# Kernel tuning notes

Hardware: AMD Instinct MI355X
Metric: run time of the kernel (lower is better)

Reference implementation:

```python
import jax, jax.numpy as jnp
import numpy as np

D = 512
K = 32
B = 2
L = 2048


def setup_inputs() -> dict:
    key = jax.random.key(0)
    ks = jax.random.split(key, 12)
    s = 1.0 / np.sqrt(D)
    return {
        "x": jax.random.normal(ks[0], (B, L, D), dtype=jnp.float32),
        "W1": jax.random.normal(ks[1], (D, D), dtype=jnp.float32) * s,
        "b1": jnp.zeros((D,), jnp.float32),
        "W2": jax.random.normal(ks[2], (D, K), dtype=jnp.float32) * s,
        "b2": jnp.zeros((K,), jnp.float32),
        "pos_scale": jnp.array([0.5], jnp.float32),
        "content_scale": jnp.array([0.5], jnp.float32),
        "Wv": jax.random.normal(ks[3], (D, D), dtype=jnp.float32) * s,
        "bv": jnp.zeros((D,), jnp.float32),
        "ln_g": jnp.ones((D,), jnp.float32),
        "ln_b": jnp.zeros((D,), jnp.float32),
        "Wo": jax.random.normal(ks[4], (D, D), dtype=jnp.float32) * s,
        "bo": jnp.zeros((D,), jnp.float32),
    }


def reference(x, W1, b1, W2, b2, pos_scale, content_scale, Wv, bv, ln_g, ln_b, Wo, bo):
    Bb, Ll, Dd = x.shape
    Kk = W2.shape[1]
    # fixed positional phases: outer(positions, 1/10000^(k/K))
    freqs = 1.0 / (10000.0 ** (jnp.arange(Kk, dtype=jnp.float32) / Kk))
    pos_phase = jnp.arange(Ll, dtype=jnp.float32)[:, None] * freqs[None, :]  # [L,K]
    # content phase: Linear -> Tanh -> Linear, then tanh * pi
    h = jnp.tanh(x @ W1 + b1)
    content_phase = jnp.tanh(h @ W2 + b2) * jnp.pi  # [B,L,K]
    total_phase = pos_scale * pos_phase[None] + content_scale * content_phase  # [B,L,K]
    value = x @ Wv + bv  # [B,L,D]
    c = jnp.cos(total_phase)
    s = jnp.sin(total_phase)
    # phasor outer-product bind: [B,L,K,D]
    bound_real = c[..., None] * value[:, :, None, :]
    bound_imag = s[..., None] * value[:, :, None, :]
    mem_real = jnp.cumsum(bound_real, axis=1)
    mem_imag = jnp.cumsum(bound_imag, axis=1)
    retrieved = (mem_real * c[..., None] + mem_imag * s[..., None]).sum(axis=2)  # [B,L,D]
    norm = jnp.sqrt(jnp.arange(1, Ll + 1, dtype=jnp.float32) * Kk)[None, :, None]
    retrieved = retrieved / norm
    # to_out: LayerNorm then Linear
    mu = retrieved.mean(axis=-1, keepdims=True)
    var = retrieved.var(axis=-1, keepdims=True)
    ln = (retrieved - mu) / jnp.sqrt(var + 1e-5) * ln_g + ln_b
    return x + ln @ Wo + bo
```

## Files before the change

### kernel.cpp

```cpp
#include <hip/hip_runtime.h>
#include <hip/hip_bf16.h>
#include <math.h>

#define BB   2
#define LL   2048
#define DD   512
#define KK   32
#define BL   (BB*LL)
#define NCH  64

typedef unsigned short ushort_t;
typedef __bf16 bf16x8 __attribute__((ext_vector_type(8)));
typedef float  f32x4  __attribute__((ext_vector_type(4)));
typedef unsigned short ushort8 __attribute__((ext_vector_type(8)));

__device__ __forceinline__ void gl_lds16(const void* g, void* l) {
    __builtin_amdgcn_global_load_lds(
        (const __attribute__((address_space(1))) void*)g,
        (__attribute__((address_space(3))) void*)l, 16, 0, 0);
}
__device__ __forceinline__ ushort_t f2b(float f) {
    __bf16 b = (__bf16)f; return *(ushort_t*)&b;
}
__device__ __forceinline__ float b2f(ushort_t u) {
    unsigned int x = ((unsigned int)u) << 16; return *(float*)&x;
}

__global__ __launch_bounds__(256) void prep(const float* __restrict__ W1,
                                            const float* __restrict__ Wv,
                                            const float* __restrict__ Wo,
                                            const float* __restrict__ W2,
                                            const float* __restrict__ x,
                                            const float* __restrict__ lng,
                                            const float* __restrict__ lnb,
                                            const float* __restrict__ bo,
                                            __hip_bfloat16* __restrict__ Wct,
                                            __hip_bfloat16* __restrict__ Wot,
                                            __hip_bfloat16* __restrict__ W2T,
                                            __hip_bfloat16* __restrict__ xb,
                                            float* __restrict__ Upart,
                                            float* __restrict__ Vpart)
{
    __shared__ float tile[32][33];
    const int bz = blockIdx.z;
    const int tx = threadIdx.x, ty = threadIdx.y;
    const int t = ty * 32 + tx;

    if (bz == 3) {
        const int bid = blockIdx.y * 16 + blockIdx.x;
        const float4* src = (const float4*)x + (size_t)bid * 2048 + t;
        ushort4* dst = (ushort4*)xb + (size_t)bid * 2048 + t;
        #pragma unroll
        for (int i = 0; i < 8; ++i) {
            float4 v = src[i * 256];
            ushort4 o = {f2b(v.x), f2b(v.y), f2b(v.z), f2b(v.w)};
            dst[i * 256] = o;
        }
        return;
    }
    if (bz == 4) {
        if (blockIdx.x != 0) return;
        const int kg = blockIdx.y;
        const int k0 = kg * 32;
        float u0 = 0.f, u1 = 0.f, v0 = 0.f, v1 = 0.f;
        #pragma unroll 4
        for (int k = 0; k < 32; ++k) {
            const float g1 = lng[k0 + k], b1v = lnb[k0 + k];
            const float w0 = Wo[(size_t)(k0 + k) * 512 + t];
            const float w1 = Wo[(size_t)(k0 + k) * 512 + t + 256];
            u0 = fmaf(g1, w0, u0);  u1 = fmaf(g1, w1, u1);
            v0 = fmaf(b1v, w0, v0); v1 = fmaf(b1v, w1, v1);
        }
        if (kg == 0) { v0 += bo[t]; v1 += bo[t + 256]; }
        Upart[kg * 512 + t] = u0;       Upart[kg * 512 + t + 256] = u1;
        Vpart[kg * 512 + t] = v0;       Vpart[kg * 512 + t + 256] = v1;
        return;
    }
    if (bz == 5) {
        if (blockIdx.x != 0) return;
        const int r0 = blockIdx.y * 32;
        #pragma unroll
        for (int i = 0; i < 4; ++i)
            tile[ty + 8 * i][tx] = W2[(size_t)(r0 + ty + 8 * i) * 32 + tx];
        __syncthreads();
        #pragma unroll
        for (int i = 0; i < 4; ++i)
            W2T[(size_t)(ty + 8 * i) * 512 + r0 + tx] =
                __float2bfloat16(tile[tx][ty + 8 * i]);
        return;
    }
    const float* src = bz == 0 ? W1 : (bz == 1 ? Wv : Wo);
    __hip_bfloat16* dst = bz == 0 ? Wct
                        : (bz == 1 ? Wct + 512 * 512 : Wot);
    const int r0 = blockIdx.y * 32, c0 = blockIdx.x * 32;
    #pragma unroll
    for (int i = 0; i < 4; ++i)
        tile[ty + 8 * i][tx] = src[(size_t)(r0 + ty + 8 * i) * 512 + c0 + tx];
    __syncthreads();
    const float sc = (bz == 2) ? lng[r0 + tx] : 1.f;
    #pragma unroll
    for (int i = 0; i < 4; ++i)
        dst[(size_t)(c0 + ty + 8 * i) * 512 + r0 + tx] =
            __float2bfloat16(tile[tx][ty + 8 * i] * sc);
}

template<int BM, int MODE>
__global__ __launch_bounds__(256) void gemm_mfma(
    const ushort_t* __restrict__ A, const ushort_t* __restrict__ Bt,
    const float* __restrict__ bias0, const float* __restrict__ bias1,
    const float* __restrict__ resid,
    __hip_bfloat16* __restrict__ outH, __hip_bfloat16* __restrict__ outV,
    float* __restrict__ outF, const float* __restrict__ stats)
{
    constexpr int WROWS = BM / 2;
    constexpr int MF    = WROWS / 16;
    constexpr int ACH   = BM / 32;
    __shared__ __align__(16) ushort_t As[BM * 64];
    __shared__ __align__(16) ushort_t Bs[128 * 64];
    __shared__ float muL[BM], rsL[BM], uL[128], vbL[128];

    const int t  = threadIdx.x;
    const int m0 = blockIdx.y * BM, n0 = blockIdx.x * 128;
    const int l  = t & 63, w = t >> 6;
    const int wr = w >> 1, wc = w & 1;
    const int l15 = l & 15, hi = l >> 4;

    if (MODE == 1) {
        if (t < BM) {
            float4 st = *(const float4*)(stats + (size_t)(m0 + t) * 4);
            float s = st.x + st.z, s2 = st.y + st.w;
            float mu = s * (1.f / 512), var = s2 * (1.f / 512) - mu * mu;
            muL[t] = mu;
            rsL[t] = rsqrtf(var + 1e-5f);
        }
        if (t < 128) {
            float u = 0.f, v = 0.f;
            #pragma unroll
            for (int kg = 0; kg < 16; ++kg) {
                u += bias0[kg * 512 + n0 + t];
                v += bias1[kg * 512 + n0 + t];
            }
            uL[t] = u; vbL[t] = v;
        }
    }

    const ushort_t* agp[ACH];
    const ushort_t* bgp[4];
    #pragma unroll
    for (int i = 0; i < ACH; ++i) {
        int row = (t >> 3) + 32 * i, slot = (t & 7) ^ (row & 7);
        agp[i] = A + (size_t)(m0 + row) * 512 + slot * 8;
    }
    #pragma unroll
    for (int i = 0; i < 4; ++i) {
        int row = (t >> 3) + 32 * i, slot = (t & 7) ^ (row & 7);
        bgp[i] = Bt + (size_t)(n0 + row) * 512 + slot * 8;
    }

    int aoff[MF][2], boff[4][2];
    #pragma unroll
    for (int mi = 0; mi < MF; ++mi)
        #pragma unroll
        for (int kh = 0; kh < 2; ++kh) {
            int row = wr * WROWS + mi * 16 + l15;
            aoff[mi][kh] = row * 128 + (((kh * 4 + hi) ^ (row & 7)) * 16);
        }
    #pragma unroll
    for (int nj = 0; nj < 4; ++nj)
        #pragma unroll
        for (int kh = 0; kh < 2; ++kh) {
            int row = wc * 64 + nj * 16 + l15;
            boff[nj][kh] = row * 128 + (((kh * 4 + hi) ^ (row & 7)) * 16);
        }

    f32x4 acc[MF][4];
    #pragma unroll
    for (int mi = 0; mi < MF; ++mi)
        #pragma unroll
        for (int nj = 0; nj < 4; ++nj)
            acc[mi][nj] = f32x4{0.f, 0.f, 0.f, 0.f};

    for (int k0 = 0; k0 < 512; k0 += 64) {
        __syncthreads();
        #pragma unroll
        for (int i = 0; i < ACH; ++i)
            gl_lds16(agp[i] + k0, (char*)As + (size_t)(i * 256 + t) * 16);
        #pragma unroll
        for (int i = 0; i < 4; ++i)
            gl_lds16(bgp[i] + k0, (char*)Bs + (size_t)(i * 256 + t) * 16);
        __syncthreads();
        #pragma unroll
        for (int kh = 0; kh < 2; ++kh) {
            bf16x8 af[MF], bfr[4];
            #pragma unroll
            for (int mi = 0; mi < MF; ++mi)
                af[mi] = *(const bf16x8*)((const char*)As + aoff[mi][kh]);
            #pragma unroll
            for (int nj = 0; nj < 4; ++nj)
                bfr[nj] = *(const bf16x8*)((const char*)Bs + boff[nj][kh]);
            #pragma unroll
            for (int mi = 0; mi < MF; ++mi)
                #pragma unroll
                for (int nj = 0; nj < 4; ++nj)
                    acc[mi][nj] = __builtin_amdgcn_mfma_f32_16x16x32_bf16(
                        af[mi], bfr[nj], acc[mi][nj], 0, 0, 0);
        }
    }

    #pragma unroll
    for (int nj = 0; nj < 4; ++nj) {
        const int gcol = n0 + wc * 64 + nj * 16 + l15;
        if (MODE == 0) {
            const float bsv = (gcol < 512) ? bias0[gcol] : bias1[gcol - 512];
            #pragma unroll
            for (int mi = 0; mi < MF; ++mi)
                #pragma unroll
                for (int r = 0; r < 4; ++r) {
                    const int grow = m0 + wr * WROWS + mi * 16 + hi * 4 + r;
                    float v = acc[mi][nj][r] + bsv;
                    if (gcol < 512)
                        outH[(size_t)grow * 512 + gcol] = __float2bfloat16(tanhf(v));
                    else
                        outV[(size_t)grow * 512 + (gcol - 512)] = __float2bfloat16(v);
                }
        } else {
            const int lc = wc * 64 + nj * 16 + l15;
            const float uN = uL[lc], vbN = vbL[lc];
            #pragma unroll
            for (int mi = 0; mi < MF; ++mi)
                #pragma unroll
                for (int r = 0; r < 4; ++r) {
                    const int rl = wr * WROWS + mi * 16 + hi * 4 + r;
                    const int grow = m0 + rl;
                    const float rs = rsL[rl], mu = muL[rl];
                    outF[(size_t)grow * 512 + gcol] =
                        resid[(size_t)grow * 512 + gcol]
                        + rs * acc[mi][nj][r] - rs * mu * uN + vbN;
                }
        }
    }
}

__global__ __launch_bounds__(256) void scanA(const __hip_bfloat16* __restrict__ Vb,
                                             const __hip_bfloat16* __restrict__ Hb,
                                             const __hip_bfloat16* __restrict__ W2T,
                                             const float* __restrict__ b2,
                                             const float* __restrict__ ps_p,
                                             const float* __restrict__ cs_p,
                                             ushort_t* __restrict__ CSg,
                                             ushort_t* __restrict__ PPg)
{
    __shared__ __align__(16) ushort_t regA[32 * 520];
    __shared__ __align__(16) ushort_t regB[32 * 520];
    ushort_t* Hs  = regA;
    ushort_t* VT  = regA;
    ushort_t* CT  = regA + 256 * 40;
    ushort_t* ST  = regA + 256 * 40 + 32 * 40;
    ushort_t* CSs = regA + 256 * 40 + 2 * 32 * 40;
    ushort_t* W2L = regB;
    ushort_t* PPs = regB;

    const int t = threadIdx.x;
    const int bch = blockIdx.x, dh = blockIdx.y;
    const int b = bch >> 6, ch = bch & 63;
    const size_t vbase = ((size_t)b * LL + ch * 32) * DD + dh * 256;
    const int w = t >> 6, l = t & 63, l15 = l & 15, hi = l >> 4;

    {
        const ushort8* hsrc = (const ushort8*)((const ushort_t*)Hb
                               + ((size_t)b * LL + ch * 32) * DD);
        const ushort8* wsrc = (const ushort8*)((const ushort_t*)W2T);
        #pragma unroll
        for (int i = 0; i < 8; ++i) {
            const int id = i * 256 + t;
            const int row = id >> 6, c8 = id & 63;
            ushort8 hv = hsrc[id];
            ushort8 wv = wsrc[id];
            *(ushort8*)&Hs[row * 520 + c8 * 8] = hv;
            *(ushort8*)&W2L[row * 520 + c8 * 8] = wv;
        }
    }
    __syncthreads();

    f32x4 pacc[2][2];
    #pragma unroll
    for (int mt = 0; mt < 2; ++mt)
        #pragma unroll
        for (int nt = 0; nt < 2; ++nt)
            pacc[mt][nt] = f32x4{0.f,0.f,0.f,0.f};
    for (int ks = 0; ks < 16; ++ks) {
        bf16x8 af[2], bfr[2];
        #pragma unroll
        for (int mt = 0; mt < 2; ++mt)
            af[mt] = *(const bf16x8*)&Hs[(16 * mt + l15) * 520 + ks * 32 + hi * 8];
        #pragma unroll
        for (int nt = 0; nt < 2; ++nt)
            bfr[nt] = *(const bf16x8*)&W2L[(16 * nt + l15) * 520 + ks * 32 + hi * 8];
        #pragma unroll
        for (int mt = 0; mt < 2; ++mt)
            #pragma unroll
            for (int nt = 0; nt < 2; ++nt)
                pacc[mt][nt] = __builtin_amdgcn_mfma_f32_16x16x32_bf16(
                    af[mt], bfr[nt], pacc[mt][nt], 0, 0, 0);
    }
    __syncthreads();

    {
        const float psv = ps_p[0], csv = cs_p[0];
        #pragma unroll
        for (int nt = 0; nt < 2; ++nt) {
            const int kk = l15 + 16 * nt;
            const float freq = exp2f(-(float)kk * (13.287712379549449f / (float)KK));
            const float b2k = b2[kk];
            #pragma unroll
            for (int mt = 0; mt < 2; ++mt) {
                ushort_t cw[4], sw[4];
                #pragma unroll
                for (int r = 0; r < 4; ++r) {
                    const int lloc = 16 * mt + hi * 4 + r;
                    const int lpos = ch * 32 + lloc;
                    const float content = tanhf(pacc[mt][nt][r] + b2k)
                                          * 3.14159265358979323846f * csv;
                    const float total = psv * ((float)lpos * freq) + content;
                    float sv, cv;
                    sincosf(total, &sv, &cv);
                    cw[r] = f2b(cv); sw[r] = f2b(sv);
                    if (dh == 0) {
                        CSs[lloc * 64 + (((kk >> 3) ^ (lloc & 7)) << 3) + (kk & 7)] = cw[r];
                        CSs[lloc * 64 + ((((kk >> 3) + 4) ^ (lloc & 7)) << 3) + (kk & 7)] = sw[r];
                    }
                }
                *(ushort4*)&CT[kk * 40 + 16 * mt + hi * 4] = *(ushort4*)cw;
                *(ushort4*)&ST[kk * 40 + 16 * mt + hi * 4] = *(ushort4*)sw;
            }
        }
    }
    {
        const int lg = t >> 5, dg = t & 31;
        ushort8 r[4];
        #pragma unroll
        for (int i = 0; i < 4; ++i)
            r[i] = *(const ushort8*)((const ushort_t*)Vb + vbase
                                     + (size_t)(lg * 4 + i) * DD + dg * 8);
        #pragma unroll
        for (int jd = 0; jd < 8; ++jd) {
            ushort4 w4 = {r[0][jd], r[1][jd], r[2][jd], r[3][jd]};
            *(ushort4*)&VT[(dg * 8 + jd) * 40 + lg * 4] = w4;
        }
    }
    __syncthreads();

    if (dh == 0) {
        ushort_t* cso = CSg + ((size_t)b * NCH + ch) * 2048;
        *(ushort8*)(cso + t * 8) = *(const ushort8*)&CSs[t * 8];
    }

    bf16x8 afc[2], afs[2];
    #pragma unroll
    for (int mt = 0; mt < 2; ++mt) {
        afc[mt] = *(const bf16x8*)&CT[(l15 + 16 * mt) * 40 + hi * 8];
        afs[mt] = *(const bf16x8*)&ST[(l15 + 16 * mt) * 40 + hi * 8];
    }
    f32x4 aPR[2][4], aPI[2][4];
    #pragma unroll
    for (int mt = 0; mt < 2; ++mt)
        #pragma unroll
        for (int nt = 0; nt < 4; ++nt) {
            aPR[mt][nt] = f32x4{0.f,0.f,0.f,0.f};
            aPI[mt][nt] = f32x4{0.f,0.f,0.f,0.f};
        }
    #pragma unroll
    for (int nt = 0; nt < 4; ++nt) {
        bf16x8 bv = *(const bf16x8*)&VT[(w * 64 + nt * 16 + l15) * 40 + hi * 8];
        #pragma unroll
        for (int mt = 0; mt < 2; ++mt) {
            aPR[mt][nt] = __builtin_amdgcn_mfma_f32_16x16x32_bf16(afc[mt], bv, aPR[mt][nt], 0,0,0);
            aPI[mt][nt] = __builtin_amdgcn_mfma_f32_16x16x32_bf16(afs[mt], bv, aPI[mt][nt], 0,0,0);
        }
    }
    #pragma unroll
    for (int mt = 0; mt < 2; ++mt)
        #pragma unroll
        for (int nt = 0; nt < 4; ++nt) {
            const int dloc = w * 64 + nt * 16 + l15;
            const int kq = 16 * mt + hi * 4;
            const int oR = kq >> 3, oI = 4 + (kq >> 3);
            const int sub = (hi & 1) * 4;
            ushort4 pr4 = {f2b(aPR[mt][nt][0]), f2b(aPR[mt][nt][1]),
                           f2b(aPR[mt][nt][2]), f2b(aPR[mt][nt][3])};
            ushort4 pi4 = {f2b(aPI[mt][nt][0]), f2b(aPI[mt][nt][1]),
                           f2b(aPI[mt][nt][2]), f2b(aPI[mt][nt][3])};
            *(ushort4*)&PPs[dloc * 64 + ((oR ^ (dloc & 7)) * 8) + sub] = pr4;
            *(ushort4*)&PPs[dloc * 64 + ((oI ^ (dloc & 7)) * 8) + sub] = pi4;
        }
    __syncthreads();
    ushort_t* gout = PPg + ((size_t)bch * 512 + dh * 256) * 64;
    #pragma unroll
    for (int i = 0; i < 8; ++i)
        *(ushort8*)(gout + (size_t)(i * 256 + t) * 8) =
            *(const ushort8*)&PPs[(i * 256 + t) * 8];
}

__global__ __launch_bounds__(256) void scan_prefix(ushort_t* __restrict__ PPg)
{
    const int g = blockIdx.x * 256 + threadIdx.x;
    const int b = g >> 15, p = g & 32767;
    float run = 0.f;
    for (int gg = 0; gg < 4; ++gg) {
        ushort_t v[16];
        #pragma unroll
        for (int i = 0; i < 16; ++i)
            v[i] = PPg[(size_t)(b * 64 + gg * 16 + i) * 32768 + p];
        #pragma unroll
        for (int i = 0; i < 16; ++i) {
            ushort_t o = f2b(run);
            run += b2f(v[i]);
            PPg[(size_t)(b * 64 + gg * 16 + i) * 32768 + p] = o;
        }
    }
}

__global__ __launch_bounds__(256) void scanC(__hip_bfloat16* Vb,
                                             const ushort_t* __restrict__ CSg,
                                             const ushort_t* __restrict__ PPg,
                                             float* __restrict__ StatsG)
{
    __shared__ __align__(16) ushort_t VT[256 * 40];
    __shared__ __align__(16) ushort_t PPT[256 * 64];
    __shared__ __align__(16) ushort_t CS[32 * 64];
    __shared__ __align__(16) ushort_t G[32 * 40];
    __shared__ __align__(16) ushort_t RT[4][32 * 64];
    __shared__ float2 statsL[4][32];

    const int t = threadIdx.x;
    const int bch = blockIdx.x, dh = blockIdx.y;
    const int b = bch >> 6, ch = bch & 63;
    const size_t vbase = ((size_t)b * LL + ch * 32) * DD + dh * 256;

    {
        const ushort_t* ppg = PPg + ((size_t)bch * 512 + dh * 256) * 64;
        #pragma unroll
        for (int i = 0; i < 8; ++i)
            gl_lds16(ppg + (size_t)(i * 256 + t) * 8,
                     (char*)PPT + (size_t)(i * 256 + t) * 16);
        const ushort_t* csg = CSg + ((size_t)b * NCH + ch) * 2048;
        gl_lds16(csg + (size_t)t * 8, (char*)CS + (size_t)t * 16);
    }
    {
        const int lg = t >> 5, dg = t & 31;
        ushort8 r[4];
        #pragma unroll
        for (int i = 0; i < 4; ++i)
            r[i] = *(const ushort8*)((const ushort_t*)Vb + vbase
                                     + (size_t)(lg * 4 + i) * DD + dg * 8);
        #pragma unroll
        for (int jd = 0; jd < 8; ++jd) {
            ushort4 w4 = {r[0][jd], r[1][jd], r[2][jd], r[3][jd]};
            *(ushort4*)&VT[(dg * 8 + jd) * 40 + lg * 4] = w4;
        }
    }
    __syncthreads();

    const int w = t >> 6, l = t & 63, l15 = l & 15, hi = l >> 4;

    bf16x8 fc[2], fs[2];
    #pragma unroll
    for (int mt = 0; mt < 2; ++mt) {
        const int row = l15 + 16 * mt;
        fc[mt] = *(const bf16x8*)&CS[row * 64 + ((hi ^ (row & 7)) << 3)];
        fs[mt] = *(const bf16x8*)&CS[row * 64 + (((4 + hi) ^ (row & 7)) << 3)];
    }

    {
        f32x4 gacc[2][2];
        #pragma unroll
        for (int mt = 0; mt < 2; ++mt)
            #pragma unroll
            for (int nt = 0; nt < 2; ++nt) {
                gacc[mt][nt] = f32x4{0.f,0.f,0.f,0.f};
                gacc[mt][nt] = __builtin_amdgcn_mfma_f32_16x16x32_bf16(fc[mt], fc[nt], gacc[mt][nt], 0,0,0);
                gacc[mt][nt] = __builtin_amdgcn_mfma_f32_16x16x32_bf16(fs[mt], fs[nt], gacc[mt][nt], 0,0,0);
            }
        #pragma unroll
        for (int mt = 0; mt < 2; ++mt)
            #pragma unroll
            for (int nt = 0; nt < 2; ++nt)
                #pragma unroll
                for (int r = 0; r < 4; ++r) {
                    const int row = 16 * mt + hi * 4 + r;
                    const int col = 16 * nt + l15;
                    float gv = (col <= row) ? gacc[mt][nt][r] : 0.f;
                    G[row * 40 + col] = f2b(gv);
                }
    }

    bf16x8 ag[2];
    #pragma unroll
    for (int mt = 0; mt < 2; ++mt)
        ag[mt] = *(const bf16x8*)&G[(l15 + 16 * mt) * 40 + hi * 8];

    f32x4 acc[2][4];
    #pragma unroll
    for (int mt = 0; mt < 2; ++mt)
        #pragma unroll
        for (int nt = 0; nt < 4; ++nt)
            acc[mt][nt] = f32x4{0.f,0.f,0.f,0.f};
    #pragma unroll
    for (int nt = 0; nt < 4; ++nt) {
        const int drow = w * 64 + nt * 16 + l15;
        bf16x8 bp0 = *(const bf16x8*)((const char*)PPT + drow * 128 + ((hi ^ (drow & 7)) << 4));
        bf16x8 bp1 = *(const bf16x8*)((const char*)PPT + drow * 128 + (((4 + hi) ^ (drow & 7)) << 4));
        bf16x8 bv  = *(const bf16x8*)&VT[drow * 40 + hi * 8];
        #pragma unroll
        for (int mt = 0; mt < 2; ++mt) {
            acc[mt][nt] = __builtin_amdgcn_mfma_f32_16x16x32_bf16(fc[mt], bp0, acc[mt][nt], 0,0,0);
            acc[mt][nt] = __builtin_amdgcn_mfma_f32_16x16x32_bf16(fs[mt], bp1, acc[mt][nt], 0,0,0);
            acc[mt][nt] = __builtin_amdgcn_mfma_f32_16x16x32_bf16(ag[mt], bv,  acc[mt][nt], 0,0,0);
        }
    }

    float sP[2][4] = {}, qP[2][4] = {};
    #pragma unroll
    for (int mt = 0; mt < 2; ++mt)
        #pragma unroll
        for (int nt = 0; nt < 4; ++nt)
            #pragma unroll
            for (int r = 0; r < 4; ++r) {
                const int lrow = 16 * mt + hi * 4 + r;
                const float scale = rsqrtf((float)((ch * 32 + lrow + 1) * KK));
                const float val = acc[mt][nt][r] * scale;
                sP[mt][r] += val;
                qP[mt][r] = fmaf(val, val, qP[mt][r]);
                RT[w][lrow * 64 + nt * 16 + l15] = f2b(val);
            }
    #pragma unroll
    for (int c = 0; c < 4; ++c) {
        const int cid = c * 64 + l;
        const int row = cid >> 3, c8 = cid & 7;
        ushort8 v = *(const ushort8*)&RT[w][row * 64 + c8 * 8];
        *(ushort8*)((ushort_t*)Vb + ((size_t)b * LL + ch * 32 + row) * DD
                    + dh * 256 + w * 64 + c8 * 8) = v;
    }
    #pragma unroll
    for (int mt = 0; mt < 2; ++mt)
        #pragma unroll
        for (int r = 0; r < 4; ++r) {
            float sv = sP[mt][r], qv = qP[mt][r];
            #pragma unroll
            for (int off = 1; off < 16; off <<= 1) {
                sv += __shfl_xor(sv, off);
                qv += __shfl_xor(qv, off);
            }
            if (l15 == 0)
                statsL[w][16 * mt + hi * 4 + r] = float2{sv, qv};
        }
    __syncthreads();
    if (t < 32) {
        float s = 0.f, q = 0.f;
        #pragma unroll
        for (int w4 = 0; w4 < 4; ++w4) {
            float2 p = statsL[w4][t];
            s += p.x; q += p.y;
        }
        const size_t rowg = (size_t)b * LL + ch * 32 + t;
        *(float2*)&StatsG[(rowg * 2 + dh) * 2] = float2{s, q};
    }
}

extern "C" void kernel_launch(void* const* d_in, const int* in_sizes, int n_in,
                              void* d_out, int out_size, void* d_ws, size_t ws_size,
                              hipStream_t stream)
{
    const float* x   = (const float*)d_in[0];
    const float* W1  = (const float*)d_in[1];
    const float* b1  = (const float*)d_in[2];
    const float* W2  = (const float*)d_in[3];
    const float* b2  = (const float*)d_in[4];
    const float* ps  = (const float*)d_in[5];
    const float* cs  = (const float*)d_in[6];
    const float* Wv  = (const float*)d_in[7];
    const float* bv  = (const float*)d_in[8];
    const float* lng = (const float*)d_in[9];
    const float* lnb = (const float*)d_in[10];
    const float* Wo  = (const float*)d_in[11];
    const float* bo  = (const float*)d_in[12];
    float* out = (float*)d_out;

    char* wsb = (char*)d_ws;
    __hip_bfloat16* Vb  = (__hip_bfloat16*)(wsb);
    ushort_t* PPg = (ushort_t*)(wsb + (4u << 20));
    ushort_t* CSg = (ushort_t*)(wsb + (12u << 20));
    __hip_bfloat16* xb  = (__hip_bfloat16*)(wsb + (13u << 20));
    __hip_bfloat16* Hb  = (__hip_bfloat16*)(wsb + (17u << 20));
    __hip_bfloat16* Wct = (__hip_bfloat16*)(wsb + (21u << 20));
    __hip_bfloat16* Wot = (__hip_bfloat16*)(wsb + (22u << 20));
    float* StatsG = (float*)(wsb + (23u << 20));
    float* Upart  = (float*)(wsb + (23u << 20) + (64u << 10));
    float* Vpart  = (float*)(wsb + (23u << 20) + (96u << 10));
    __hip_bfloat16* W2T = (__hip_bfloat16*)(wsb + (23u << 20) + (128u << 10));

    prep<<<dim3(16, 16, 6), dim3(32, 8), 0, stream>>>(
        W1, Wv, Wo, W2, x, lng, lnb, bo, Wct, Wot, W2T, xb, Upart, Vpart);
    gemm_mfma<64, 0><<<dim3(8, 64), dim3(256), 0, stream>>>(
        (const ushort_t*)xb, (const ushort_t*)Wct, b1, bv, nullptr, Hb, Vb, nullptr, nullptr);
    scanA<<<dim3(BB * NCH, 2), dim3(256), 0, stream>>>(
        Vb, Hb, W2T, b2, ps, cs, CSg, PPg);
    scan_prefix<<<dim3(256), dim3(256), 0, stream>>>(PPg);
    scanC<<<dim3(BB * NCH, 2), dim3(256), 0, stream>>>(Vb, CSg, PPg, StatsG);
    gemm_mfma<32, 1><<<dim3(4, 128), dim3(256), 0, stream>>>(
        (const ushort_t*)Vb, (const ushort_t*)Wot, Upart, Vpart, x, nullptr, nullptr, out, StatsG);
}
```

Measured before the change: 59.91 us.

## Double-buffer GEMM LDS tiles and swizzle transposed V tiles in scan kernels

The MFMA GEMM now keeps two LDS buffers for the A and B tiles and issues global-to-LDS loads for the next k-slice before computing on the current one. This removes one barrier per iteration and overlaps loads with MFMA work. The scan kernels change the transposed V tile from a padded stride of 40 to a stride of 64 with an XOR swizzle, which is meant to cut LDS bank conflicts. The final scan kernel reuses the VT buffer for its output staging after an extra barrier, in place of a separate RT array. LDS use per block goes up in the GEMM, which may lower occupancy, and the correctness of the single-barrier double buffer depends on global_load_lds completion ordering.

```diff
diff --git a/kernel.cpp b/kernel.cpp
--- a/kernel.cpp
+++ b/kernel.cpp
@@ -115,8 +115,8 @@
     constexpr int WROWS = BM / 2;
     constexpr int MF    = WROWS / 16;
     constexpr int ACH   = BM / 32;
-    __shared__ __align__(16) ushort_t As[BM * 64];
-    __shared__ __align__(16) ushort_t Bs[128 * 64];
+    __shared__ __align__(16) ushort_t As[2][BM * 64];
+    __shared__ __align__(16) ushort_t Bs[2][128 * 64];
     __shared__ float muL[BM], rsL[BM], uL[128], vbL[128];
 
     const int t  = threadIdx.x;
@@ -180,24 +180,30 @@
         for (int nj = 0; nj < 4; ++nj)
             acc[mi][nj] = f32x4{0.f, 0.f, 0.f, 0.f};
 
-    for (int k0 = 0; k0 < 512; k0 += 64) {
+    auto stage = [&](int bs, int k0) {
+        #pragma unroll
+        for (int i = 0; i < ACH; ++i)
+            gl_lds16(agp[i] + k0, (char*)As[bs] + (size_t)(i * 256 + t) * 16);
+        #pragma unroll
+        for (int i = 0; i < 4; ++i)
+            gl_lds16(bgp[i] + k0, (char*)Bs[bs] + (size_t)(i * 256 + t) * 16);
+    };
+
+    stage(0, 0);
+    for (int ks = 0; ks < 8; ++ks) {
         __syncthreads();
-        #pragma unroll
-        for (int i = 0; i < ACH; ++i)
-            gl_lds16(agp[i] + k0, (char*)As + (size_t)(i * 256 + t) * 16);
-        #pragma unroll
-        for (int i = 0; i < 4; ++i)
-            gl_lds16(bgp[i] + k0, (char*)Bs + (size_t)(i * 256 + t) * 16);
-        __syncthreads();
+        if (ks < 7) stage((ks + 1) & 1, (ks + 1) * 64);
+        const char* as = (const char*)As[ks & 1];
+        const char* bsp = (const char*)Bs[ks & 1];
         #pragma unroll
         for (int kh = 0; kh < 2; ++kh) {
             bf16x8 af[MF], bfr[4];
             #pragma unroll
             for (int mi = 0; mi < MF; ++mi)
-                af[mi] = *(const bf16x8*)((const char*)As + aoff[mi][kh]);
+                af[mi] = *(const bf16x8*)(as + aoff[mi][kh]);
             #pragma unroll
             for (int nj = 0; nj < 4; ++nj)
-                bfr[nj] = *(const bf16x8*)((const char*)Bs + boff[nj][kh]);
+                bfr[nj] = *(const bf16x8*)(bsp + boff[nj][kh]);
             #pragma unroll
             for (int mi = 0; mi < MF; ++mi)
                 #pragma unroll
@@ -241,6 +247,7 @@
     }
 }
 
+
 __global__ __launch_bounds__(256) void scanA(const __hip_bfloat16* __restrict__ Vb,
                                              const __hip_bfloat16* __restrict__ Hb,
                                              const __hip_bfloat16* __restrict__ W2T,
@@ -250,13 +257,13 @@
                                              ushort_t* __restrict__ CSg,
                                              ushort_t* __restrict__ PPg)
 {
-    __shared__ __align__(16) ushort_t regA[32 * 520];
+    __shared__ __align__(16) ushort_t regA[256 * 64 + 2 * 32 * 40 + 32 * 64];
     __shared__ __align__(16) ushort_t regB[32 * 520];
     ushort_t* Hs  = regA;
     ushort_t* VT  = regA;
-    ushort_t* CT  = regA + 256 * 40;
-    ushort_t* ST  = regA + 256 * 40 + 32 * 40;
-    ushort_t* CSs = regA + 256 * 40 + 2 * 32 * 40;
+    ushort_t* CT  = regA + 256 * 64;
+    ushort_t* ST  = regA + 256 * 64 + 32 * 40;
+    ushort_t* CSs = regA + 256 * 64 + 2 * 32 * 40;
     ushort_t* W2L = regB;
     ushort_t* PPs = regB;
 
@@ -342,10 +349,12 @@
         for (int i = 0; i < 4; ++i)
             r[i] = *(const ushort8*)((const ushort_t*)Vb + vbase
                                      + (size_t)(lg * 4 + i) * DD + dg * 8);
+        const int oct = (lg >> 1) ^ (dg & 7);
+        const int sub = (lg & 1) * 4;
         #pragma unroll
         for (int jd = 0; jd < 8; ++jd) {
             ushort4 w4 = {r[0][jd], r[1][jd], r[2][jd], r[3][jd]};
-            *(ushort4*)&VT[(dg * 8 + jd) * 40 + lg * 4] = w4;
+            *(ushort4*)&VT[(dg * 8 + jd) * 64 + oct * 8 + sub] = w4;
         }
     }
     __syncthreads();
@@ -371,7 +380,8 @@
         }
     #pragma unroll
     for (int nt = 0; nt < 4; ++nt) {
-        bf16x8 bv = *(const bf16x8*)&VT[(w * 64 + nt * 16 + l15) * 40 + hi * 8];
+        const int drow = w * 64 + nt * 16 + l15;
+        bf16x8 bv = *(const bf16x8*)&VT[drow * 64 + ((hi ^ ((drow >> 3) & 7)) << 3)];
         #pragma unroll
         for (int mt = 0; mt < 2; ++mt) {
             aPR[mt][nt] = __builtin_amdgcn_mfma_f32_16x16x32_bf16(afc[mt], bv, aPR[mt][nt], 0,0,0);
@@ -425,11 +435,10 @@
                                              const ushort_t* __restrict__ PPg,
                                              float* __restrict__ StatsG)
 {
-    __shared__ __align__(16) ushort_t VT[256 * 40];
+    __shared__ __align__(16) ushort_t VT[256 * 64];
     __shared__ __align__(16) ushort_t PPT[256 * 64];
     __shared__ __align__(16) ushort_t CS[32 * 64];
     __shared__ __align__(16) ushort_t G[32 * 40];
-    __shared__ __align__(16) ushort_t RT[4][32 * 64];
     __shared__ float2 statsL[4][32];
 
     const int t = threadIdx.x;
@@ -453,10 +462,12 @@
         for (int i = 0; i < 4; ++i)
             r[i] = *(const ushort8*)((const ushort_t*)Vb + vbase
                                      + (size_t)(lg * 4 + i) * DD + dg * 8);
+        const int oct = (lg >> 1) ^ (dg & 7);
+        const int sub = (lg & 1) * 4;
         #pragma unroll
         for (int jd = 0; jd < 8; ++jd) {
             ushort4 w4 = {r[0][jd], r[1][jd], r[2][jd], r[3][jd]};
-            *(ushort4*)&VT[(dg * 8 + jd) * 40 + lg * 4] = w4;
+            *(ushort4*)&VT[(dg * 8 + jd) * 64 + oct * 8 + sub] = w4;
         }
     }
     __syncthreads();
@@ -510,7 +521,7 @@
         const int drow = w * 64 + nt * 16 + l15;
         bf16x8 bp0 = *(const bf16x8*)((const char*)PPT + drow * 128 + ((hi ^ (drow & 7)) << 4));
         bf16x8 bp1 = *(const bf16x8*)((const char*)PPT + drow * 128 + (((4 + hi) ^ (drow & 7)) << 4));
-        bf16x8 bv  = *(const bf16x8*)&VT[drow * 40 + hi * 8];
+        bf16x8 bv  = *(const bf16x8*)&VT[drow * 64 + ((hi ^ ((drow >> 3) & 7)) << 3)];
         #pragma unroll
         for (int mt = 0; mt < 2; ++mt) {
             acc[mt][nt] = __builtin_amdgcn_mfma_f32_16x16x32_bf16(fc[mt], bp0, acc[mt][nt], 0,0,0);
@@ -518,6 +529,9 @@
             acc[mt][nt] = __builtin_amdgcn_mfma_f32_16x16x32_bf16(ag[mt], bv,  acc[mt][nt], 0,0,0);
         }
     }
+
+    __syncthreads();
+    ushort_t* RTw = VT + w * 2048;
 
     float sP[2][4] = {}, qP[2][4] = {};
     #pragma unroll
@@ -531,13 +545,13 @@
                 const float val = acc[mt][nt][r] * scale;
                 sP[mt][r] += val;
                 qP[mt][r] = fmaf(val, val, qP[mt][r]);
-                RT[w][lrow * 64 + nt * 16 + l15] = f2b(val);
+                RTw[lrow * 64 + nt * 16 + l15] = f2b(val);
             }
     #pragma unroll
     for (int c = 0; c < 4; ++c) {
         const int cid = c * 64 + l;
         const int row = cid >> 3, c8 = cid & 7;
-        ushort8 v = *(const ushort8*)&RT[w][row * 64 + c8 * 8];
+        ushort8 v = *(const ushort8*)&RTw[row * 64 + c8 * 8];
         *(ushort8*)((ushort_t*)Vb + ((size_t)b * LL + ch * 32 + row) * DD
                     + dh * 256 + w * 64 + c8 * 8) = v;
     }
```

Result: slower. 61.23 us (+2.2%).
